# Performance work log

Measured on AMD Instinct MI355X. Metric: run time of the kernel, lower is better.

Reference implementation:

```python
import jax, jax.numpy as jnp
import numpy as np

IOU_THRESHOLD = 0.5
MIN_SIZE = 16.0
SCORE_THRESHOLD = 0.5
MAX_PROPOSALS = 300


def setup_inputs() -> dict:
    key = jax.random.key(0)
    k_c, k_wh, k_s = jax.random.split(key, 3)
    B, N = 8, 4000
    # realistic boxes: x1<x2, y1<y2, sizes straddling min_size=16
    cxcy = jax.random.uniform(k_c, (B, N, 2), minval=0.0, maxval=800.0)
    wh = jax.random.uniform(k_wh, (B, N, 2), minval=4.0, maxval=256.0)
    proposals = jnp.concatenate([cxcy - wh / 2, cxcy + wh / 2], axis=-1)
    cls_scores = jax.random.uniform(k_s, (B, N, 2))
    return {"proposals": proposals, "cls_scores": cls_scores}


def _pairwise_iou(boxes):
    # boxes: [N,4] -> iou [N,N]
    x1, y1, x2, y2 = boxes[:, 0], boxes[:, 1], boxes[:, 2], boxes[:, 3]
    area = (x2 - x1) * (y2 - y1)
    xi1 = jnp.maximum(x1[:, None], x1[None, :])
    yi1 = jnp.maximum(y1[:, None], y1[None, :])
    xi2 = jnp.minimum(x2[:, None], x2[None, :])
    yi2 = jnp.minimum(y2[:, None], y2[None, :])
    inter = jnp.clip(xi2 - xi1, 0.0) * jnp.clip(yi2 - yi1, 0.0)
    union = area[:, None] + area[None, :] - inter
    return inter / union


def _filter_one(boxes, scores2):
    # boxes [N,4], scores2 [N,2]
    fg = scores2[:, 1]
    w = boxes[:, 2] - boxes[:, 0]
    h = boxes[:, 3] - boxes[:, 1]
    valid = (fg > SCORE_THRESHOLD) & (w >= MIN_SIZE) & (h >= MIN_SIZE)
    # sort by score descending; invalid boxes pushed to the end
    order = jnp.argsort(-jnp.where(valid, fg, -jnp.inf))
    b = boxes[order]
    valid = valid[order]
    N = b.shape[0]
    # selection is non-differentiable; stop grads through the IoU graph
    iou = jax.lax.stop_gradient(_pairwise_iou(b))
    ar = jnp.arange(N)

    def body(i, keep):
        # if box i is kept, suppress all later boxes with IoU >= threshold
        # (original drops ious < thr -> suppressed when iou >= thr)
        sup = keep[i] & (iou[i] >= IOU_THRESHOLD) & (ar > i)
        return keep & ~sup

    keep = jax.lax.fori_loop(0, N, body, valid)
    # scatter kept boxes (in score order) into fixed [MAX_PROPOSALS,4], zero-padded
    rank = jnp.cumsum(keep) - 1
    pos = jnp.where(keep, jnp.minimum(rank, MAX_PROPOSALS), MAX_PROPOSALS)
    out = jnp.zeros((MAX_PROPOSALS + 1, 4), b.dtype).at[pos].set(b)
    return out[:MAX_PROPOSALS]


def reference(proposals, cls_scores):
    # [B, MAX_PROPOSALS, 4], zero-padded where fewer boxes survive
    return jax.vmap(_filter_one)(proposals, cls_scores)
```

## Files before the change

kernel.cpp:

```cpp
#include <hip/hip_runtime.h>

#define NBOX 4000
#define NPAD 4096
#define BATCH 8
#define WPR 64
#define MAXK 300

typedef unsigned long long u64;

__device__ u64 g_sup[BATCH][NPAD][WPR];
__device__ u64 g_tile64[BATCH][64][64];
__device__ u64 g_colT[BATCH][65][64];
__device__ float4 g_sorted[BATCH][NPAD];
__device__ int g_nvalid[BATCH];

#define SORT_T 1024
#define EPT 4
#define HP2 1088

__global__ __launch_bounds__(SORT_T) void sort_kernel(const float* __restrict__ props,
                                                      const float* __restrict__ scores) {
    const int b = blockIdx.x;
    const int tid = threadIdx.x;
    __shared__ unsigned int K0[NPAD], K1[NPAD];
    __shared__ unsigned short P0[NPAD], P1[NPAD];
    __shared__ unsigned short Hs[16 * HP2];
    __shared__ unsigned int sWT[16];
    __shared__ int s_cnt;
    if (tid == 0) s_cnt = 0;
    __syncthreads();

    int localc = 0;
    {
        const int n0 = tid * EPT;
        unsigned int kk[EPT];
        #pragma unroll
        for (int e = 0; e < EPT; ++e) {
            const int n = n0 + e;
            unsigned int k = 0xFFFFFFu;
            if (n < NBOX) {
                const float2 sc = *reinterpret_cast<const float2*>(scores + ((size_t)b * NBOX + n) * 2);
                const float4 p  = *reinterpret_cast<const float4*>(props  + ((size_t)b * NBOX + n) * 4);
                const float fg = sc.y;
                const float w = __fsub_rn(p.z, p.x);
                const float h = __fsub_rn(p.w, p.y);
                if ((fg > 0.5f) && (w >= 16.0f) && (h >= 16.0f)) {
                    k = 0x3F800000u - __float_as_uint(fg);
                    localc++;
                }
            }
            kk[e] = k;
        }
        *reinterpret_cast<uint4*>(&K0[n0]) = make_uint4(kk[0], kk[1], kk[2], kk[3]);
        ushort4 pp;
        pp.x = (unsigned short)(n0 + 0); pp.y = (unsigned short)(n0 + 1);
        pp.z = (unsigned short)(n0 + 2); pp.w = (unsigned short)(n0 + 3);
        *reinterpret_cast<ushort4*>(&P0[n0]) = pp;
    }
    for (int off = 32; off > 0; off >>= 1) localc += __shfl_down(localc, off);
    if ((tid & 63) == 0) atomicAdd(&s_cnt, localc);

    unsigned int kr[EPT];
    unsigned short pr[EPT];

    for (int pass = 0; pass < 6; ++pass) {
        const int shift = pass * 4;
        const unsigned int*   ksrc = (pass & 1) ? K1 : K0;
        unsigned int*         kdst = (pass & 1) ? K0 : K1;
        const unsigned short* psrc = (pass & 1) ? P1 : P0;
        unsigned short*       pdst = (pass & 1) ? P0 : P1;

        for (int hh = tid; hh < (16 * HP2) / 2; hh += SORT_T)
            reinterpret_cast<unsigned int*>(Hs)[hh] = 0;
        __syncthreads();

        {
            const uint4 kv = *reinterpret_cast<const uint4*>(&ksrc[tid * EPT]);
            kr[0] = kv.x; kr[1] = kv.y; kr[2] = kv.z; kr[3] = kv.w;
            const ushort4 pv = *reinterpret_cast<const ushort4*>(&psrc[tid * EPT]);
            pr[0] = pv.x; pr[1] = pv.y; pr[2] = pv.z; pr[3] = pv.w;
        }
        #pragma unroll
        for (int e = 0; e < EPT; ++e) {
            const unsigned int d = (kr[e] >> shift) & 15u;
            Hs[d * HP2 + tid]++;
        }
        __syncthreads();

        {
            const int d  = tid >> 6;
            const int t0 = (tid & 63) * 16;
            unsigned short* row = &Hs[d * HP2];
            unsigned int sum = 0;
            #pragma unroll
            for (int e = 0; e < 16; ++e) {
                const unsigned int v = row[t0 + e];
                row[t0 + e] = (unsigned short)sum;
                sum += v;
            }
            unsigned int x = sum;
            #pragma unroll
            for (int off = 1; off < 64; off <<= 1) {
                const unsigned int y = __shfl_up(x, off);
                if ((tid & 63) >= off) x += y;
            }
            const int wid = tid >> 6;
            if ((tid & 63) == 63) sWT[wid] = x;
            __syncthreads();
            unsigned int base = x - sum;
            for (int w = 0; w < wid; ++w) base += sWT[w];
            #pragma unroll
            for (int e = 0; e < 16; ++e) row[t0 + e] += (unsigned short)base;
        }
        __syncthreads();

        #pragma unroll
        for (int e = 0; e < EPT; ++e) {
            const unsigned int d = (kr[e] >> shift) & 15u;
            const unsigned int pos = Hs[d * HP2 + tid]++;
            kdst[pos] = kr[e];
            pdst[pos] = pr[e];
        }
        __syncthreads();
    }

    const int nv = s_cnt;
    if (tid == 0) g_nvalid[b] = nv;
    {
        const int p0 = tid * EPT;
        const ushort4 pv = *reinterpret_cast<const ushort4*>(&P0[p0]);
        const unsigned short pe[EPT] = {pv.x, pv.y, pv.z, pv.w};
        #pragma unroll
        for (int e = 0; e < EPT; ++e) {
            const int p = p0 + e;
            if (p < nv)
                g_sorted[b][p] = *reinterpret_cast<const float4*>(props + ((size_t)b * NBOX + pe[e]) * 4);
        }
    }
}

__global__ __launch_bounds__(64) void iou_kernel() {
    const int id = blockIdx.x;
    const int b = id & (BATCH - 1);
    const int i = id >> 3;
    const int nv = g_nvalid[b];
    if (i >= nv) return;
    const int lane = threadIdx.x;
    const int c0 = i >> 6;
    const int W = (nv + 63) >> 6;

    const float4 bi = g_sorted[b][i];
    const float areai = __fmul_rn(__fsub_rn(bi.z, bi.x), __fsub_rn(bi.w, bi.y));

    u64 myword = 0ull;
    for (int c = c0; c < W; ++c) {
        const int j = (c << 6) + lane;
        bool pred = false;
        if (j < nv && j > i) {
            const float4 bj = g_sorted[b][j];
            const float areaj = __fmul_rn(__fsub_rn(bj.z, bj.x), __fsub_rn(bj.w, bj.y));
            const float xi1 = fmaxf(bi.x, bj.x);
            const float yi1 = fmaxf(bi.y, bj.y);
            const float xi2 = fminf(bi.z, bj.z);
            const float yi2 = fminf(bi.w, bj.w);
            const float iw = fmaxf(__fsub_rn(xi2, xi1), 0.0f);
            const float ih = fmaxf(__fsub_rn(yi2, yi1), 0.0f);
            const float inter = __fmul_rn(iw, ih);
            const float uni = __fsub_rn(__fadd_rn(areai, areaj), inter);
            pred = (inter / uni) >= 0.5f;
        }
        const u64 wd = __ballot(pred);
        if (lane == c) myword = wd;
    }
    g_sup[b][i][lane] = myword;
    if (lane == c0) g_tile64[b][c0][i & 63] = myword;
}

__global__ __launch_bounds__(64) void colT_kernel() {
    const int id = blockIdx.x;
    const int b = id & (BATCH - 1);
    const int t = id >> 3;
    const int j = threadIdx.x;
    const u64* rw = &g_tile64[b][t][0];
    u64 col = 0ull;
    #pragma unroll
    for (int r = 0; r < 64; ++r)
        col |= ((rw[r] >> j) & 1ull) << r;
    g_colT[b][t][j] = col;
}

__device__ __forceinline__ unsigned int rdlu(unsigned int v, int l) {
    return (unsigned int)__builtin_amdgcn_readlane((int)v, l);
}
__device__ __forceinline__ u64 rdl64(u64 v, int l) {
    const unsigned lo = rdlu((unsigned)v, l);
    const unsigned hi = rdlu((unsigned)(v >> 32), l);
    return ((u64)hi << 32) | lo;
}

__global__ __launch_bounds__(64) void nms_kernel(float* __restrict__ out) {
    const int b = blockIdx.x;
    const int lane = threadIdx.x;
    int nv = g_nvalid[b];
    if (nv > NBOX) nv = NBOX;
    float4* outv = reinterpret_cast<float4*>(out) + (size_t)b * MAXK;
    const u64* supb = &g_sup[b][0][0];
    __shared__ int sIdx[64];

    for (int s = lane; s < MAXK; s += 64)
        outv[s] = make_float4(0.0f, 0.0f, 0.0f, 0.0f);

    u64 removed = 0ull;
    int kept = 0;
    const int nblk = (nv + 63) >> 6;

    u64 colT = g_colT[b][0][lane];

    for (int blk = 0; blk < nblk && kept < MAXK; ++blk) {
        const int base = blk << 6;
        const u64 colT_n = g_colT[b][blk + 1][lane];

        const u64 wv = rdl64(removed, blk);
        const int alive = (int)((~wv >> lane) & 1ull) & (int)(base + lane < nv);

        u64 bal = __ballot(alive != 0);
        const unsigned cLo = (unsigned)colT, cHi = (unsigned)(colT >> 32);
        while (bal != 0ull) {
            const unsigned bLo = (unsigned)bal, bHi = (unsigned)(bal >> 32);
            const int sup = (((cLo & bLo) | (cHi & bHi)) != 0u);
            const u64 nb = __ballot((alive & (sup ^ 1)) != 0);
            if (nb == bal) break;
            bal = nb;
        }

        int m = __popcll(bal);
        const int cap = MAXK - kept;
        while (m > cap) {
            bal &= ~(1ull << (63 - __builtin_clzll(bal)));
            --m;
        }

        if (m > 0) {
            unsigned rank = __builtin_amdgcn_mbcnt_lo((unsigned)bal, 0u);
            rank = __builtin_amdgcn_mbcnt_hi((unsigned)(bal >> 32), rank);
            if ((bal >> lane) & 1ull) sIdx[rank] = base + lane;
            const int myIdx = sIdx[lane];
            if (lane < m) outv[kept + lane] = g_sorted[b][myIdx];

            if (kept + m < MAXK && blk + 1 < nblk) {
                u64 balT = bal;
                for (int t = 0; t < m; t += 32) {
#define LDW(j) u64 v##j = 0ull; {                                               \
                        if (t + j < m) {                                        \
                            const int it = base + __builtin_ctzll(balT);        \
                            balT &= balT - 1ull;                                \
                            v##j = supb[(size_t)it * WPR + lane];               \
                        } }
                    LDW(0)  LDW(1)  LDW(2)  LDW(3)  LDW(4)  LDW(5)  LDW(6)  LDW(7)
                    LDW(8)  LDW(9)  LDW(10) LDW(11) LDW(12) LDW(13) LDW(14) LDW(15)
                    LDW(16) LDW(17) LDW(18) LDW(19) LDW(20) LDW(21) LDW(22) LDW(23)
                    LDW(24) LDW(25) LDW(26) LDW(27) LDW(28) LDW(29) LDW(30) LDW(31)
#undef LDW
                    const u64 o0 = ((v0 | v1) | (v2 | v3)) | ((v4 | v5) | (v6 | v7));
                    const u64 o1 = ((v8 | v9) | (v10 | v11)) | ((v12 | v13) | (v14 | v15));
                    const u64 o2 = ((v16 | v17) | (v18 | v19)) | ((v20 | v21) | (v22 | v23));
                    const u64 o3 = ((v24 | v25) | (v26 | v27)) | ((v28 | v29) | (v30 | v31));
                    removed |= (o0 | o1) | (o2 | o3);
                }
            }
            kept += m;
        }
        colT = colT_n;
    }
}

extern "C" void kernel_launch(void* const* d_in, const int* in_sizes, int n_in,
                              void* d_out, int out_size, void* d_ws, size_t ws_size,
                              hipStream_t stream) {
    const float* props  = (const float*)d_in[0];
    const float* scores = (const float*)d_in[1];
    float* out = (float*)d_out;

    sort_kernel<<<BATCH, SORT_T, 0, stream>>>(props, scores);
    iou_kernel<<<NBOX * BATCH, 64, 0, stream>>>();
    colT_kernel<<<64 * BATCH, 64, 0, stream>>>();
    nms_kernel<<<BATCH, 64, 0, stream>>>(out);
}
```

Before: 63.75 us.

## Fold column-transpose into IoU kernel via atomics, precompute areas, pad sorted boxes

Removes the separate colT kernel launch by having the IoU kernel build the transposed diagonal tile directly with atomicOr, and the sort kernel now zeroes g_colT. Box areas are precomputed once in the sort kernel, and unused slots are filled with far-away sentinel boxes so the IoU inner loop drops its bounds branch. The NMS suppression gather reads kept indices from shared memory instead of walking the ballot mask serially. The costs are contended atomics on the diagonal tile, extra global writes for padding and areas, and redundant clamped loads when fewer than 32 boxes are kept.

```diff
diff --git a/kernel.cpp b/kernel.cpp
--- a/kernel.cpp
+++ b/kernel.cpp
@@ -9,9 +9,9 @@
 typedef unsigned long long u64;
 
 __device__ u64 g_sup[BATCH][NPAD][WPR];
-__device__ u64 g_tile64[BATCH][64][64];
 __device__ u64 g_colT[BATCH][65][64];
 __device__ float4 g_sorted[BATCH][NPAD];
+__device__ float g_area[BATCH][NPAD];
 __device__ int g_nvalid[BATCH];
 
 #define SORT_T 1024
@@ -133,10 +133,18 @@
         #pragma unroll
         for (int e = 0; e < EPT; ++e) {
             const int p = p0 + e;
-            if (p < nv)
-                g_sorted[b][p] = *reinterpret_cast<const float4*>(props + ((size_t)b * NBOX + pe[e]) * 4);
-        }
-    }
+            if (p < nv) {
+                const float4 bx = *reinterpret_cast<const float4*>(props + ((size_t)b * NBOX + pe[e]) * 4);
+                g_sorted[b][p] = bx;
+                g_area[b][p] = __fmul_rn(__fsub_rn(bx.z, bx.x), __fsub_rn(bx.w, bx.y));
+            } else {
+                g_sorted[b][p] = make_float4(2e9f, 2e9f, 2e9f, 2e9f);
+                g_area[b][p] = 0.0f;
+            }
+        }
+    }
+    for (int z = tid; z < 65 * 64; z += SORT_T)
+        (&g_colT[b][0][0])[z] = 0ull;
 }
 
 __global__ __launch_bounds__(64) void iou_kernel() {
@@ -150,43 +158,44 @@
     const int W = (nv + 63) >> 6;
 
     const float4 bi = g_sorted[b][i];
-    const float areai = __fmul_rn(__fsub_rn(bi.z, bi.x), __fsub_rn(bi.w, bi.y));
+    const float areai = g_area[b][i];
 
     u64 myword = 0ull;
-    for (int c = c0; c < W; ++c) {
+    {
+        const int j = (c0 << 6) + lane;
+        const float4 bj = g_sorted[b][j];
+        const float areaj = g_area[b][j];
+        const float xi1 = fmaxf(bi.x, bj.x);
+        const float yi1 = fmaxf(bi.y, bj.y);
+        const float xi2 = fminf(bi.z, bj.z);
+        const float yi2 = fminf(bi.w, bj.w);
+        const float iw = fmaxf(__fsub_rn(xi2, xi1), 0.0f);
+        const float ih = fmaxf(__fsub_rn(yi2, yi1), 0.0f);
+        const float inter = __fmul_rn(iw, ih);
+        const float uni = __fsub_rn(__fadd_rn(areai, areaj), inter);
+        const bool pred = ((inter / uni) >= 0.5f) && (j > i);
+        const u64 wd = __ballot(pred);
+        if (lane == c0) myword = wd;
+        const u64 contrib = ((wd >> lane) & 1ull) << (i & 63);
+        if (contrib) atomicOr(&g_colT[b][c0][lane], contrib);
+    }
+    for (int c = c0 + 1; c < W; ++c) {
         const int j = (c << 6) + lane;
-        bool pred = false;
-        if (j < nv && j > i) {
-            const float4 bj = g_sorted[b][j];
-            const float areaj = __fmul_rn(__fsub_rn(bj.z, bj.x), __fsub_rn(bj.w, bj.y));
-            const float xi1 = fmaxf(bi.x, bj.x);
-            const float yi1 = fmaxf(bi.y, bj.y);
-            const float xi2 = fminf(bi.z, bj.z);
-            const float yi2 = fminf(bi.w, bj.w);
-            const float iw = fmaxf(__fsub_rn(xi2, xi1), 0.0f);
-            const float ih = fmaxf(__fsub_rn(yi2, yi1), 0.0f);
-            const float inter = __fmul_rn(iw, ih);
-            const float uni = __fsub_rn(__fadd_rn(areai, areaj), inter);
-            pred = (inter / uni) >= 0.5f;
-        }
+        const float4 bj = g_sorted[b][j];
+        const float areaj = g_area[b][j];
+        const float xi1 = fmaxf(bi.x, bj.x);
+        const float yi1 = fmaxf(bi.y, bj.y);
+        const float xi2 = fminf(bi.z, bj.z);
+        const float yi2 = fminf(bi.w, bj.w);
+        const float iw = fmaxf(__fsub_rn(xi2, xi1), 0.0f);
+        const float ih = fmaxf(__fsub_rn(yi2, yi1), 0.0f);
+        const float inter = __fmul_rn(iw, ih);
+        const float uni = __fsub_rn(__fadd_rn(areai, areaj), inter);
+        const bool pred = (inter / uni) >= 0.5f;
         const u64 wd = __ballot(pred);
         if (lane == c) myword = wd;
     }
     g_sup[b][i][lane] = myword;
-    if (lane == c0) g_tile64[b][c0][i & 63] = myword;
-}
-
-__global__ __launch_bounds__(64) void colT_kernel() {
-    const int id = blockIdx.x;
-    const int b = id & (BATCH - 1);
-    const int t = id >> 3;
-    const int j = threadIdx.x;
-    const u64* rw = &g_tile64[b][t][0];
-    u64 col = 0ull;
-    #pragma unroll
-    for (int r = 0; r < 64; ++r)
-        col |= ((rw[r] >> j) & 1ull) << r;
-    g_colT[b][t][j] = col;
 }
 
 __device__ __forceinline__ unsigned int rdlu(unsigned int v, int l) {
@@ -248,14 +257,11 @@
             if (lane < m) outv[kept + lane] = g_sorted[b][myIdx];
 
             if (kept + m < MAXK && blk + 1 < nblk) {
-                u64 balT = bal;
                 for (int t = 0; t < m; t += 32) {
-#define LDW(j) u64 v##j = 0ull; {                                               \
-                        if (t + j < m) {                                        \
-                            const int it = base + __builtin_ctzll(balT);        \
-                            balT &= balT - 1ull;                                \
-                            v##j = supb[(size_t)it * WPR + lane];               \
-                        } }
+#define LDW(j) u64 v##j; {                                                      \
+                        int tt = t + j; if (tt >= m) tt = m - 1;                \
+                        const int it = sIdx[tt];                                \
+                        v##j = supb[(size_t)it * WPR + lane];                   }
                     LDW(0)  LDW(1)  LDW(2)  LDW(3)  LDW(4)  LDW(5)  LDW(6)  LDW(7)
                     LDW(8)  LDW(9)  LDW(10) LDW(11) LDW(12) LDW(13) LDW(14) LDW(15)
                     LDW(16) LDW(17) LDW(18) LDW(19) LDW(20) LDW(21) LDW(22) LDW(23)
@@ -283,6 +289,5 @@
 
     sort_kernel<<<BATCH, SORT_T, 0, stream>>>(props, scores);
     iou_kernel<<<NBOX * BATCH, 64, 0, stream>>>();
-    colT_kernel<<<64 * BATCH, 64, 0, stream>>>();
     nms_kernel<<<BATCH, 64, 0, stream>>>(out);
 }
```

After: 59.58 us. -6.5%, faster.
